# Optimization experiments

Hardware: AMD Instinct MI355X
Metric: run time of the kernel (lower is better)

Reference implementation:

```python
import jax, jax.numpy as jnp
import numpy as np

Z, Y, X = 41, 1024, 1024   # spatial_shape (z, y, x)
N = 300000                 # active voxels
C_IN, C_OUT, K = 32, 64, 3


def setup_inputs() -> dict:
    key = jax.random.key(0)
    k1, k2 = jax.random.split(key)
    # unique active voxel coordinates (spconv indices layout: [batch, z, y, x])
    rng = np.random.default_rng(0)
    lin = rng.choice(Z * Y * X, size=N, replace=False)
    z = lin // (Y * X)
    y = (lin // X) % Y
    x = lin % X
    indices = np.stack([np.zeros(N, np.int64), z, y, x], axis=1).astype(np.int32)
    features = jax.random.normal(k1, (N, C_IN), dtype=jnp.float32)
    fan_in = K * K * K * C_IN
    weight = jax.random.normal(k2, (K * K * K, C_IN, C_OUT), dtype=jnp.float32) / np.sqrt(fan_in)
    return {"features": features, "indices": jnp.asarray(indices), "weight": weight}


def reference(features, indices, weight):
    """Submanifold sparse 3D conv (SubMConv3d, k=3, pad=1, no bias).

    Output sites == input active sites. For each of the 27 kernel offsets:
    look up the neighbor voxel in a dense coordinate hash, gather its
    features, matmul with that offset's [C_in, C_out] weight slice, and
    accumulate (gather-matmul-scatter rulebook form).
    """
    n = features.shape[0]
    zc, yc, xc = indices[:, 1], indices[:, 2], indices[:, 3]
    lin = (zc * (Y * X) + yc * X + xc).astype(jnp.int32)
    # dense hash: linear voxel coord -> row in `features`, -1 if inactive
    grid = jnp.full((Z * Y * X,), -1, dtype=jnp.int32).at[lin].set(
        jnp.arange(n, dtype=jnp.int32))

    out = jnp.zeros((n, C_OUT), dtype=features.dtype)
    k = 0
    for dz in (-1, 0, 1):
        for dy in (-1, 0, 1):
            for dx in (-1, 0, 1):
                nz, ny, nx = zc + dz, yc + dy, xc + dx
                inb = ((nz >= 0) & (nz < Z) & (ny >= 0) & (ny < Y)
                       & (nx >= 0) & (nx < X))
                nlin = jnp.where(inb, nz * (Y * X) + ny * X + nx, 0)
                nidx = grid[nlin]                       # [N] row or -1
                mask = inb & (nidx >= 0)
                feat = features[jnp.where(mask, nidx, 0)]
                feat = feat * mask[:, None].astype(features.dtype)
                out = out + feat @ weight[k]            # [N,Cin]@[Cin,Cout]
                k += 1
    return out
```

## Files before the change

### kernel.cpp

```cpp
#include <hip/hip_runtime.h>
#include <hip/hip_fp16.h>


#define ZD 41
#define YD 1024
#define XD 1024

constexpr int CIN = 32;
constexpr int COUT = 64;
constexpr unsigned HASH_BITS = 20;
constexpr unsigned CAP = 1u << HASH_BITS;
constexpr unsigned GROUP_BITS = HASH_BITS - 3;
constexpr unsigned long long EMPTY = ~0ull;
constexpr unsigned NVOX = ZD * YD * XD;
constexpr unsigned NOCT = NVOX / 8;
constexpr unsigned BMWORDS = (NOCT + 31) / 32;
constexpr int PPW = 16;
constexpr int CAND_CAP = 96;
constexpr int HROWS = 48;
constexpr int WPACK_N = 27 * 4 * 64;

typedef _Float16 half2_t __attribute__((ext_vector_type(2)));
typedef _Float16 half8_t __attribute__((ext_vector_type(8)));
typedef __fp16 pk2_t __attribute__((ext_vector_type(2)));
typedef float floatx4 __attribute__((ext_vector_type(4)));

union H2U { pk2_t p; half2_t h; unsigned u; };
union H8U { half8_t v; half2_t h2[4]; pk2_t p2[4]; uint4 u4; };

__host__ __device__ constexpr unsigned pack6(int k) {
    return (unsigned)((k % 3) | (((k / 3) % 3) << 2) | ((k / 9) << 4));
}
__host__ __device__ constexpr unsigned cw_round(int t) {
    unsigned w = 0;
    for (int j4 = 0; j4 < 4; ++j4) {
        int off = 4 * t + j4;
        if (off < 26) {
            int k = off + (off >= 13);
            w |= pack6(k) << (6 * j4);
        }
    }
    return w;
}

__device__ __forceinline__ unsigned hash_slot(unsigned lin) {
    unsigned gh = ((lin >> 3) * 2654435761u) >> (32 - GROUP_BITS);
    return (gh << 3) | (lin & 7u);
}

__global__ void build_hash_kernel(const int4* __restrict__ idx, int n,
                                  unsigned long long* __restrict__ table,
                                  unsigned* __restrict__ bitmap,
                                  const float* __restrict__ weight,
                                  uint4* __restrict__ wpack) {
    int i = blockIdx.x * blockDim.x + threadIdx.x;
    if (i < WPACK_N) {
        int co = i & 63, g = (i >> 6) & 3, k = i >> 8;
        const float* b = weight + k * (CIN * COUT) + (8 * g) * COUT + co;
        H2U p0, p1, p2, p3;
        p0.p = __builtin_amdgcn_cvt_pkrtz(b[0 * COUT], b[1 * COUT]);
        p1.p = __builtin_amdgcn_cvt_pkrtz(b[2 * COUT], b[3 * COUT]);
        p2.p = __builtin_amdgcn_cvt_pkrtz(b[4 * COUT], b[5 * COUT]);
        p3.p = __builtin_amdgcn_cvt_pkrtz(b[6 * COUT], b[7 * COUT]);
        wpack[i] = make_uint4(p0.u, p1.u, p2.u, p3.u);
    }
    if (i >= n) return;
    int4 c = idx[i];
    unsigned lin = (unsigned)(c.y * (YD * XD) + c.z * XD + c.w);
    unsigned g = lin >> 3;
    atomicAnd(&bitmap[g >> 5], ~(1u << (g & 31u)));
    unsigned long long packed = ((unsigned long long)(unsigned)i << 32) | (unsigned long long)lin;
    unsigned h = hash_slot(lin);
    while (atomicCAS(&table[h], EMPTY, packed) != EMPTY) {
        h = (h + 1) & (CAP - 1);
    }
}

__device__ __forceinline__ int lookup(const unsigned long long* __restrict__ table,
                                      unsigned lin) {
    unsigned h = hash_slot(lin);
    while (true) {
        unsigned long long s = table[h];
        if (s == EMPTY) return -1;
        if ((unsigned)s == lin) return (int)(s >> 32);
        h = (h + 1) & (CAP - 1);
    }
}

__device__ __forceinline__ void fb_tap(const float* __restrict__ feat,
                                       const float* __restrict__ weight,
                                       float* __restrict__ acc,
                                       int ni, int pt, int k, int lane) {
    const float4* fr = (const float4*)(feat + (size_t)ni * CIN);
    const float* wk = weight + k * (CIN * COUT) + lane;
    float s0 = 0.f, s1 = 0.f, s2 = 0.f, s3 = 0.f;
#pragma unroll
    for (int q = 0; q < 8; ++q) {
        float4 f = fr[q];
        s0 = fmaf(f.x, wk[(4 * q + 0) * COUT], s0);
        s1 = fmaf(f.y, wk[(4 * q + 1) * COUT], s1);
        s2 = fmaf(f.z, wk[(4 * q + 2) * COUT], s2);
        s3 = fmaf(f.w, wk[(4 * q + 3) * COUT], s3);
    }
    acc[pt * COUT + lane] += (s0 + s1) + (s2 + s3);
}

__global__ __launch_bounds__(256, 4) void subm_conv_kernel(
    const float* __restrict__ feat, const int4* __restrict__ idx,
    const float* __restrict__ weight, const uint4* __restrict__ wpack,
    const unsigned long long* __restrict__ table,
    const unsigned* __restrict__ bitmap, float* __restrict__ out, int n) {
    __shared__ unsigned rows_l[4][HROWS * 16];
    __shared__ float accum_l[4][PPW * COUT];
    __shared__ unsigned long long cand_l[4][CAND_CAP];
    __shared__ unsigned hlist_l[4][HROWS];

    int wid = threadIdx.x >> 6;
    int lane = threadIdx.x & 63;
    int p0 = (blockIdx.x * 4 + wid) * PPW;
    if (p0 >= n) return;
    int np = min(PPW, n - p0);

    int pt = lane >> 2;
    int4 c = idx[p0 + (pt < np ? pt : 0)];

    int sh6 = (lane & 3) * 6;
    bool ptok = (pt < np);
    unsigned nlin_t[7];
    unsigned bmw[7];
    bool try_t[7];
#pragma unroll
    for (int t = 0; t < 7; ++t) {
        unsigned w = (cw_round(t) >> sh6) & 63u;
        int nz = c.y + (int)(w >> 4) - 1;
        int ny = c.z + (int)((w >> 2) & 3u) - 1;
        int nx = c.w + (int)(w & 3u) - 1;
        bool ok = ptok && (unsigned)nz < (unsigned)ZD && (unsigned)ny < (unsigned)YD &&
                  (unsigned)nx < (unsigned)XD;
        if (t == 6) ok = ok && ((lane & 3) < 2);
        unsigned nlin = ok ? ((((unsigned)nz << 10) + (unsigned)ny) << 10) + (unsigned)nx : 0u;
        nlin_t[t] = nlin;
        try_t[t] = ok;
        bmw[t] = ok ? bitmap[nlin >> 8] : ~0u;
    }

    int arow = lane & 15, aq = lane >> 4;
    int rowp = p0 + (arow < np ? arow : np - 1);
    float4 af0 = *(const float4*)(feat + (size_t)rowp * CIN + aq * 8);
    float4 af1 = *(const float4*)(feat + (size_t)rowp * CIN + aq * 8 + 4);
    H8U afrag;
    afrag.p2[0] = __builtin_amdgcn_cvt_pkrtz(af0.x, af0.y);
    afrag.p2[1] = __builtin_amdgcn_cvt_pkrtz(af0.z, af0.w);
    afrag.p2[2] = __builtin_amdgcn_cvt_pkrtz(af1.x, af1.y);
    afrag.p2[3] = __builtin_amdgcn_cvt_pkrtz(af1.z, af1.w);

    floatx4 cacc[4];
#pragma unroll
    for (int ch = 0; ch < 4; ++ch) {
        H8U bfrag;
        bfrag.u4 = wpack[(13 * 4 + aq) * 64 + ch * 16 + (lane & 15)];
        floatx4 z = {0.f, 0.f, 0.f, 0.f};
        cacc[ch] = __builtin_amdgcn_mfma_f32_16x16x32_f16(afrag.v, bfrag.v, z, 0, 0, 0);
    }
#pragma unroll
    for (int ch = 0; ch < 4; ++ch) {
#pragma unroll
        for (int r = 0; r < 4; ++r) {
            accum_l[wid][((lane >> 4) * 4 + r) * COUT + ch * 16 + (lane & 15)] = cacc[ch][r];
        }
    }

    int cbase = 0;
    unsigned ovmask = 0;
#pragma unroll
    for (int t = 0; t < 7; ++t) {
        unsigned nlin = nlin_t[t];
        bool candq = try_t[t] && !((bmw[t] >> ((nlin >> 3) & 31u)) & 1u);
        unsigned long long m = __ballot(candq);
        if (candq) {
            int r = cbase + __popcll(m & ((1ull << lane) - 1ull));
            int off = (lane & 3) + 4 * t;
            int k = off + (off >= 13);
            if (r < CAND_CAP) {
                cand_l[wid][r] = ((unsigned long long)(((unsigned)pt << 5) | (unsigned)k) << 32)
                                 | (unsigned long long)nlin;
            } else {
                ovmask |= 1u << t;
            }
        }
        cbase += __popcll(m);
    }
    int ncand = cbase < CAND_CAP ? cbase : CAND_CAP;
    __asm__ __volatile__("s_waitcnt lgkmcnt(0)" ::: "memory");

    int hitbase = 0;
    int hni[2];
    unsigned hmeta[2];
    bool hov[2] = {false, false};
#pragma unroll
    for (int sub = 0; sub < 2; ++sub) {
        int j = sub * 64 + lane;
        int ni = -1;
        unsigned meta = 0;
        if (j < ncand) {
            unsigned long long e = cand_l[wid][j];
            meta = (unsigned)(e >> 32);
            ni = lookup(table, (unsigned)e);
        }
        unsigned long long m = __ballot(ni >= 0);
        if (ni >= 0) {
            int hr = hitbase + __popcll(m & ((1ull << lane) - 1ull));
            if (hr < HROWS) {
                hlist_l[wid][hr] = ((unsigned)ni << 9) | meta;
            } else {
                hov[sub] = true; hni[sub] = ni; hmeta[sub] = meta;
            }
        }
        hitbase += __popcll(m);
    }
    int hits = hitbase < HROWS ? hitbase : HROWS;
    __asm__ __volatile__("s_waitcnt lgkmcnt(0)" ::: "memory");

    for (int e = lane; e < hits * 4; e += 64) {
        int r = e >> 2, s = e & 3;
        int ni = (int)(hlist_l[wid][r] >> 9);
        float4 u = *(const float4*)(feat + (size_t)ni * CIN + s * 8);
        float4 v = *(const float4*)(feat + (size_t)ni * CIN + s * 8 + 4);
        H2U q0, q1, q2, q3;
        q0.p = __builtin_amdgcn_cvt_pkrtz(u.x, u.y);
        q1.p = __builtin_amdgcn_cvt_pkrtz(u.z, u.w);
        q2.p = __builtin_amdgcn_cvt_pkrtz(v.x, v.y);
        q3.p = __builtin_amdgcn_cvt_pkrtz(v.z, v.w);
        *(uint4*)&rows_l[wid][r * 16 + s * 4] = make_uint4(q0.u, q1.u, q2.u, q3.u);
    }
    __asm__ __volatile__("s_waitcnt vmcnt(0) lgkmcnt(0)" ::: "memory");

    for (int j = 0; j < hits; ++j) {
        unsigned meta = hlist_l[wid][j] & 511u;
        int k = (int)(meta & 31u);
        int pt2 = (int)(meta >> 5);
        float s = 0.f;
#pragma unroll
        for (int g = 0; g < 4; ++g) {
            H8U fv, wv;
            fv.u4 = *(const uint4*)&rows_l[wid][j * 16 + g * 4];
            wv.u4 = wpack[(k * 4 + g) * 64 + lane];
            s = __builtin_amdgcn_fdot2(fv.h2[0], wv.h2[0], s, false);
            s = __builtin_amdgcn_fdot2(fv.h2[1], wv.h2[1], s, false);
            s = __builtin_amdgcn_fdot2(fv.h2[2], wv.h2[2], s, false);
            s = __builtin_amdgcn_fdot2(fv.h2[3], wv.h2[3], s, false);
        }
        accum_l[wid][pt2 * COUT + lane] += s;
    }

    if (__builtin_expect(cbase > CAND_CAP, 0)) {
#pragma unroll
        for (int t = 0; t < 7; ++t) {
            unsigned long long m = __ballot((ovmask >> t) & 1u);
            while (m) {
                int src = __ffsll((unsigned long long)m) - 1;
                m &= m - 1;
                unsigned nlin = __shfl(nlin_t[t], src);
                int pt2 = src >> 2;
                int off = (src & 3) + 4 * t;
                int k = off + (off >= 13);
                int ni = lookup(table, nlin);
                if (ni >= 0) fb_tap(feat, weight, accum_l[wid], ni, pt2, k, lane);
            }
        }
    }
    if (__builtin_expect(hitbase > HROWS, 0)) {
#pragma unroll
        for (int sub = 0; sub < 2; ++sub) {
            unsigned long long m = __ballot(hov[sub]);
            while (m) {
                int src = __ffsll((unsigned long long)m) - 1;
                m &= m - 1;
                int ni = __shfl(hni[sub], src);
                unsigned meta = (unsigned)__shfl((int)hmeta[sub], src);
                fb_tap(feat, weight, accum_l[wid], ni, (int)((meta >> 5) & 15u),
                       (int)(meta & 31u), lane);
            }
        }
    }
    __asm__ __volatile__("s_waitcnt lgkmcnt(0)" ::: "memory");

    for (int e = lane; e < np * 16; e += 64) {
        int g = e >> 4, cq = e & 15;
        floatx4 v = *(const floatx4*)&accum_l[wid][g * COUT + cq * 4];
        __builtin_nontemporal_store(v, (floatx4*)&out[(size_t)(p0 + g) * COUT + cq * 4]);
    }
}

extern "C" void kernel_launch(void* const* d_in, const int* in_sizes, int n_in,
                              void* d_out, int out_size, void* d_ws, size_t ws_size,
                              hipStream_t stream) {
    const float* feat   = (const float*)d_in[0];
    const int4*  idx    = (const int4*)d_in[1];
    const float* weight = (const float*)d_in[2];
    float* out = (float*)d_out;
    int n = in_sizes[0] / CIN;

    unsigned char* base = (unsigned char*)d_ws;
    unsigned long long* table = (unsigned long long*)base;
    unsigned* bitmap = (unsigned*)(base + (size_t)CAP * 8);
    uint4* wpack = (uint4*)(base + (size_t)CAP * 8 + (size_t)BMWORDS * 4);

    hipMemsetAsync(table, 0xFF, (size_t)CAP * 8 + (size_t)BMWORDS * 4, stream);

    int bwork = n > WPACK_N ? n : WPACK_N;
    int bblocks = (bwork + 255) / 256;
    build_hash_kernel<<<bblocks, 256, 0, stream>>>(idx, n, table, bitmap, weight, wpack);

    int ppb = 4 * PPW;
    int cblocks = (n + ppb - 1) / ppb;
    subm_conv_kernel<<<cblocks, 256, 0, stream>>>(feat, idx, weight, wpack, table,
                                                  bitmap, out, n);
}
```

Before: 184.0 us.

## Make conv kernel persistent and prefetch next group's coordinates and bitmap words

Converts the per-wave single-group kernel into a grid-stride persistent loop capped at a fixed block count. Coordinates and occupancy-bitmap words for the next group are loaded and computed while the current group does its hash lookups and gathers, hiding their latency. It also removes the vmcnt wait before the dot-product loop. The cap reduces resident waves per CU, which may lower latency hiding for the gather-heavy path, and adds register pressure from the carried prefetch state.

Result: slower. 209.3 us (+13.8%).

```diff
diff --git a/kernel.cpp b/kernel.cpp
--- a/kernel.cpp
+++ b/kernel.cpp
@@ -19,6 +19,7 @@
 constexpr int CAND_CAP = 96;
 constexpr int HROWS = 48;
 constexpr int WPACK_N = 27 * 4 * 64;
+constexpr int PERSIST_BLOCKS = 768;
 
 typedef _Float16 half2_t __attribute__((ext_vector_type(2)));
 typedef _Float16 half8_t __attribute__((ext_vector_type(8)));
@@ -117,178 +118,222 @@
 
     int wid = threadIdx.x >> 6;
     int lane = threadIdx.x & 63;
-    int p0 = (blockIdx.x * 4 + wid) * PPW;
-    if (p0 >= n) return;
-    int np = min(PPW, n - p0);
-
     int pt = lane >> 2;
-    int4 c = idx[p0 + (pt < np ? pt : 0)];
-
     int sh6 = (lane & 3) * 6;
-    bool ptok = (pt < np);
-    unsigned nlin_t[7];
-    unsigned bmw[7];
-    bool try_t[7];
-#pragma unroll
-    for (int t = 0; t < 7; ++t) {
-        unsigned w = (cw_round(t) >> sh6) & 63u;
-        int nz = c.y + (int)(w >> 4) - 1;
-        int ny = c.z + (int)((w >> 2) & 3u) - 1;
-        int nx = c.w + (int)(w & 3u) - 1;
-        bool ok = ptok && (unsigned)nz < (unsigned)ZD && (unsigned)ny < (unsigned)YD &&
-                  (unsigned)nx < (unsigned)XD;
-        if (t == 6) ok = ok && ((lane & 3) < 2);
-        unsigned nlin = ok ? ((((unsigned)nz << 10) + (unsigned)ny) << 10) + (unsigned)nx : 0u;
-        nlin_t[t] = nlin;
-        try_t[t] = ok;
-        bmw[t] = ok ? bitmap[nlin >> 8] : ~0u;
-    }
-
-    int arow = lane & 15, aq = lane >> 4;
-    int rowp = p0 + (arow < np ? arow : np - 1);
-    float4 af0 = *(const float4*)(feat + (size_t)rowp * CIN + aq * 8);
-    float4 af1 = *(const float4*)(feat + (size_t)rowp * CIN + aq * 8 + 4);
-    H8U afrag;
-    afrag.p2[0] = __builtin_amdgcn_cvt_pkrtz(af0.x, af0.y);
-    afrag.p2[1] = __builtin_amdgcn_cvt_pkrtz(af0.z, af0.w);
-    afrag.p2[2] = __builtin_amdgcn_cvt_pkrtz(af1.x, af1.y);
-    afrag.p2[3] = __builtin_amdgcn_cvt_pkrtz(af1.z, af1.w);
-
-    floatx4 cacc[4];
-#pragma unroll
-    for (int ch = 0; ch < 4; ++ch) {
-        H8U bfrag;
-        bfrag.u4 = wpack[(13 * 4 + aq) * 64 + ch * 16 + (lane & 15)];
-        floatx4 z = {0.f, 0.f, 0.f, 0.f};
-        cacc[ch] = __builtin_amdgcn_mfma_f32_16x16x32_f16(afrag.v, bfrag.v, z, 0, 0, 0);
-    }
-#pragma unroll
-    for (int ch = 0; ch < 4; ++ch) {
-#pragma unroll
-        for (int r = 0; r < 4; ++r) {
-            accum_l[wid][((lane >> 4) * 4 + r) * COUT + ch * 16 + (lane & 15)] = cacc[ch][r];
-        }
-    }
-
-    int cbase = 0;
-    unsigned ovmask = 0;
-#pragma unroll
-    for (int t = 0; t < 7; ++t) {
-        unsigned nlin = nlin_t[t];
-        bool candq = try_t[t] && !((bmw[t] >> ((nlin >> 3) & 31u)) & 1u);
-        unsigned long long m = __ballot(candq);
-        if (candq) {
-            int r = cbase + __popcll(m & ((1ull << lane) - 1ull));
-            int off = (lane & 3) + 4 * t;
-            int k = off + (off >= 13);
-            if (r < CAND_CAP) {
-                cand_l[wid][r] = ((unsigned long long)(((unsigned)pt << 5) | (unsigned)k) << 32)
-                                 | (unsigned long long)nlin;
-            } else {
-                ovmask |= 1u << t;
-            }
-        }
-        cbase += __popcll(m);
-    }
-    int ncand = cbase < CAND_CAP ? cbase : CAND_CAP;
-    __asm__ __volatile__("s_waitcnt lgkmcnt(0)" ::: "memory");
-
-    int hitbase = 0;
-    int hni[2];
-    unsigned hmeta[2];
-    bool hov[2] = {false, false};
-#pragma unroll
-    for (int sub = 0; sub < 2; ++sub) {
-        int j = sub * 64 + lane;
-        int ni = -1;
-        unsigned meta = 0;
-        if (j < ncand) {
-            unsigned long long e = cand_l[wid][j];
-            meta = (unsigned)(e >> 32);
-            ni = lookup(table, (unsigned)e);
-        }
-        unsigned long long m = __ballot(ni >= 0);
-        if (ni >= 0) {
-            int hr = hitbase + __popcll(m & ((1ull << lane) - 1ull));
-            if (hr < HROWS) {
-                hlist_l[wid][hr] = ((unsigned)ni << 9) | meta;
-            } else {
-                hov[sub] = true; hni[sub] = ni; hmeta[sub] = meta;
-            }
-        }
-        hitbase += __popcll(m);
-    }
-    int hits = hitbase < HROWS ? hitbase : HROWS;
-    __asm__ __volatile__("s_waitcnt lgkmcnt(0)" ::: "memory");
-
-    for (int e = lane; e < hits * 4; e += 64) {
-        int r = e >> 2, s = e & 3;
-        int ni = (int)(hlist_l[wid][r] >> 9);
-        float4 u = *(const float4*)(feat + (size_t)ni * CIN + s * 8);
-        float4 v = *(const float4*)(feat + (size_t)ni * CIN + s * 8 + 4);
-        H2U q0, q1, q2, q3;
-        q0.p = __builtin_amdgcn_cvt_pkrtz(u.x, u.y);
-        q1.p = __builtin_amdgcn_cvt_pkrtz(u.z, u.w);
-        q2.p = __builtin_amdgcn_cvt_pkrtz(v.x, v.y);
-        q3.p = __builtin_amdgcn_cvt_pkrtz(v.z, v.w);
-        *(uint4*)&rows_l[wid][r * 16 + s * 4] = make_uint4(q0.u, q1.u, q2.u, q3.u);
-    }
-    __asm__ __volatile__("s_waitcnt vmcnt(0) lgkmcnt(0)" ::: "memory");
-
-    for (int j = 0; j < hits; ++j) {
-        unsigned meta = hlist_l[wid][j] & 511u;
-        int k = (int)(meta & 31u);
-        int pt2 = (int)(meta >> 5);
-        float s = 0.f;
-#pragma unroll
-        for (int g = 0; g < 4; ++g) {
-            H8U fv, wv;
-            fv.u4 = *(const uint4*)&rows_l[wid][j * 16 + g * 4];
-            wv.u4 = wpack[(k * 4 + g) * 64 + lane];
-            s = __builtin_amdgcn_fdot2(fv.h2[0], wv.h2[0], s, false);
-            s = __builtin_amdgcn_fdot2(fv.h2[1], wv.h2[1], s, false);
-            s = __builtin_amdgcn_fdot2(fv.h2[2], wv.h2[2], s, false);
-            s = __builtin_amdgcn_fdot2(fv.h2[3], wv.h2[3], s, false);
-        }
-        accum_l[wid][pt2 * COUT + lane] += s;
-    }
-
-    if (__builtin_expect(cbase > CAND_CAP, 0)) {
+
+    int ngroups = (n + PPW - 1) / PPW;
+    int gstride = gridDim.x * 4;
+    int g = blockIdx.x * 4 + wid;
+    if (g >= ngroups) return;
+
+    unsigned nlin_n[7], bmw_n[7];
+    bool try_n[7];
+    {
+        int np0 = min(PPW, n - g * PPW);
+        int4 cc = idx[g * PPW + (pt < np0 ? pt : 0)];
+        bool ptok = (pt < np0);
 #pragma unroll
         for (int t = 0; t < 7; ++t) {
-            unsigned long long m = __ballot((ovmask >> t) & 1u);
-            while (m) {
-                int src = __ffsll((unsigned long long)m) - 1;
-                m &= m - 1;
-                unsigned nlin = __shfl(nlin_t[t], src);
-                int pt2 = src >> 2;
-                int off = (src & 3) + 4 * t;
+            unsigned w = (cw_round(t) >> sh6) & 63u;
+            int nz = cc.y + (int)(w >> 4) - 1;
+            int ny = cc.z + (int)((w >> 2) & 3u) - 1;
+            int nx = cc.w + (int)(w & 3u) - 1;
+            bool ok = ptok && (unsigned)nz < (unsigned)ZD && (unsigned)ny < (unsigned)YD &&
+                      (unsigned)nx < (unsigned)XD;
+            if (t == 6) ok = ok && ((lane & 3) < 2);
+            unsigned nl = ok ? ((((unsigned)nz << 10) + (unsigned)ny) << 10) + (unsigned)nx : 0u;
+            nlin_n[t] = nl;
+            try_n[t] = ok;
+            bmw_n[t] = ok ? bitmap[nl >> 8] : ~0u;
+        }
+    }
+
+    for (; g < ngroups; g += gstride) {
+        int p0 = g * PPW;
+        int np = min(PPW, n - p0);
+
+        unsigned nlin_t[7], bmw[7];
+        bool try_t[7];
+#pragma unroll
+        for (int t = 0; t < 7; ++t) {
+            nlin_t[t] = nlin_n[t];
+            bmw[t] = bmw_n[t];
+            try_t[t] = try_n[t];
+        }
+
+        int gn = g + gstride;
+        bool has_next = gn < ngroups;
+        int np_nx = has_next ? min(PPW, n - gn * PPW) : np;
+        int nsrc = has_next ? (gn * PPW + (pt < np_nx ? pt : 0)) : p0;
+        int4 cnext = idx[nsrc];
+
+        int arow = lane & 15, aq = lane >> 4;
+        int rowp = p0 + (arow < np ? arow : np - 1);
+        float4 af0 = *(const float4*)(feat + (size_t)rowp * CIN + aq * 8);
+        float4 af1 = *(const float4*)(feat + (size_t)rowp * CIN + aq * 8 + 4);
+        H8U afrag;
+        afrag.p2[0] = __builtin_amdgcn_cvt_pkrtz(af0.x, af0.y);
+        afrag.p2[1] = __builtin_amdgcn_cvt_pkrtz(af0.z, af0.w);
+        afrag.p2[2] = __builtin_amdgcn_cvt_pkrtz(af1.x, af1.y);
+        afrag.p2[3] = __builtin_amdgcn_cvt_pkrtz(af1.z, af1.w);
+
+        floatx4 cacc[4];
+#pragma unroll
+        for (int ch = 0; ch < 4; ++ch) {
+            H8U bfrag;
+            bfrag.u4 = wpack[(13 * 4 + aq) * 64 + ch * 16 + (lane & 15)];
+            floatx4 z = {0.f, 0.f, 0.f, 0.f};
+            cacc[ch] = __builtin_amdgcn_mfma_f32_16x16x32_f16(afrag.v, bfrag.v, z, 0, 0, 0);
+        }
+#pragma unroll
+        for (int ch = 0; ch < 4; ++ch) {
+#pragma unroll
+            for (int r = 0; r < 4; ++r) {
+                accum_l[wid][((lane >> 4) * 4 + r) * COUT + ch * 16 + (lane & 15)] =
+                    cacc[ch][r];
+            }
+        }
+
+        int cbase = 0;
+        unsigned ovmask = 0;
+#pragma unroll
+        for (int t = 0; t < 7; ++t) {
+            unsigned nlin = nlin_t[t];
+            bool candq = try_t[t] && !((bmw[t] >> ((nlin >> 3) & 31u)) & 1u);
+            unsigned long long m = __ballot(candq);
+            if (candq) {
+                int r = cbase + __popcll(m & ((1ull << lane) - 1ull));
+                int off = (lane & 3) + 4 * t;
                 int k = off + (off >= 13);
-                int ni = lookup(table, nlin);
-                if (ni >= 0) fb_tap(feat, weight, accum_l[wid], ni, pt2, k, lane);
-            }
-        }
-    }
-    if (__builtin_expect(hitbase > HROWS, 0)) {
+                if (r < CAND_CAP) {
+                    cand_l[wid][r] =
+                        ((unsigned long long)(((unsigned)pt << 5) | (unsigned)k) << 32)
+                        | (unsigned long long)nlin;
+                } else {
+                    ovmask |= 1u << t;
+                }
+            }
+            cbase += __popcll(m);
+        }
+        int ncand = cbase < CAND_CAP ? cbase : CAND_CAP;
+        __asm__ __volatile__("s_waitcnt lgkmcnt(0)" ::: "memory");
+
+        int hitbase = 0;
+        int hni[2];
+        unsigned hmeta[2];
+        bool hov[2] = {false, false};
 #pragma unroll
         for (int sub = 0; sub < 2; ++sub) {
-            unsigned long long m = __ballot(hov[sub]);
-            while (m) {
-                int src = __ffsll((unsigned long long)m) - 1;
-                m &= m - 1;
-                int ni = __shfl(hni[sub], src);
-                unsigned meta = (unsigned)__shfl((int)hmeta[sub], src);
-                fb_tap(feat, weight, accum_l[wid], ni, (int)((meta >> 5) & 15u),
-                       (int)(meta & 31u), lane);
-            }
-        }
-    }
-    __asm__ __volatile__("s_waitcnt lgkmcnt(0)" ::: "memory");
-
-    for (int e = lane; e < np * 16; e += 64) {
-        int g = e >> 4, cq = e & 15;
-        floatx4 v = *(const floatx4*)&accum_l[wid][g * COUT + cq * 4];
-        __builtin_nontemporal_store(v, (floatx4*)&out[(size_t)(p0 + g) * COUT + cq * 4]);
+            int j = sub * 64 + lane;
+            int ni = -1;
+            unsigned meta = 0;
+            if (j < ncand) {
+                unsigned long long e = cand_l[wid][j];
+                meta = (unsigned)(e >> 32);
+                ni = lookup(table, (unsigned)e);
+            }
+            unsigned long long m = __ballot(ni >= 0);
+            if (ni >= 0) {
+                int hr = hitbase + __popcll(m & ((1ull << lane) - 1ull));
+                if (hr < HROWS) {
+                    hlist_l[wid][hr] = ((unsigned)ni << 9) | meta;
+                } else {
+                    hov[sub] = true; hni[sub] = ni; hmeta[sub] = meta;
+                }
+            }
+            hitbase += __popcll(m);
+        }
+        int hits = hitbase < HROWS ? hitbase : HROWS;
+        __asm__ __volatile__("s_waitcnt lgkmcnt(0)" ::: "memory");
+
+        {
+            bool ptok_n = has_next && (pt < np_nx);
+#pragma unroll
+            for (int t = 0; t < 7; ++t) {
+                unsigned w = (cw_round(t) >> sh6) & 63u;
+                int nz = cnext.y + (int)(w >> 4) - 1;
+                int ny = cnext.z + (int)((w >> 2) & 3u) - 1;
+                int nx = cnext.w + (int)(w & 3u) - 1;
+                bool ok = ptok_n && (unsigned)nz < (unsigned)ZD &&
+                          (unsigned)ny < (unsigned)YD && (unsigned)nx < (unsigned)XD;
+                if (t == 6) ok = ok && ((lane & 3) < 2);
+                unsigned nl = ok ? ((((unsigned)nz << 10) + (unsigned)ny) << 10) + (unsigned)nx
+                                 : 0u;
+                nlin_n[t] = nl;
+                try_n[t] = ok;
+                bmw_n[t] = ok ? bitmap[nl >> 8] : ~0u;
+            }
+        }
+
+        for (int e = lane; e < hits * 4; e += 64) {
+            int r = e >> 2, s = e & 3;
+            int ni = (int)(hlist_l[wid][r] >> 9);
+            float4 u = *(const float4*)(feat + (size_t)ni * CIN + s * 8);
+            float4 v = *(const float4*)(feat + (size_t)ni * CIN + s * 8 + 4);
+            H2U q0, q1, q2, q3;
+            q0.p = __builtin_amdgcn_cvt_pkrtz(u.x, u.y);
+            q1.p = __builtin_amdgcn_cvt_pkrtz(u.z, u.w);
+            q2.p = __builtin_amdgcn_cvt_pkrtz(v.x, v.y);
+            q3.p = __builtin_amdgcn_cvt_pkrtz(v.z, v.w);
+            *(uint4*)&rows_l[wid][r * 16 + s * 4] = make_uint4(q0.u, q1.u, q2.u, q3.u);
+        }
+        __asm__ __volatile__("s_waitcnt lgkmcnt(0)" ::: "memory");
+
+        for (int j = 0; j < hits; ++j) {
+            unsigned meta = hlist_l[wid][j] & 511u;
+            int k = (int)(meta & 31u);
+            int pt2 = (int)(meta >> 5);
+            float s = 0.f;
+#pragma unroll
+            for (int gg = 0; gg < 4; ++gg) {
+                H8U fv, wv;
+                fv.u4 = *(const uint4*)&rows_l[wid][j * 16 + gg * 4];
+                wv.u4 = wpack[(k * 4 + gg) * 64 + lane];
+                s = __builtin_amdgcn_fdot2(fv.h2[0], wv.h2[0], s, false);
+                s = __builtin_amdgcn_fdot2(fv.h2[1], wv.h2[1], s, false);
+                s = __builtin_amdgcn_fdot2(fv.h2[2], wv.h2[2], s, false);
+                s = __builtin_amdgcn_fdot2(fv.h2[3], wv.h2[3], s, false);
+            }
+            accum_l[wid][pt2 * COUT + lane] += s;
+        }
+
+        if (__builtin_expect(cbase > CAND_CAP, 0)) {
+#pragma unroll
+            for (int t = 0; t < 7; ++t) {
+                unsigned long long m = __ballot((ovmask >> t) & 1u);
+                while (m) {
+                    int src = __ffsll((unsigned long long)m) - 1;
+                    m &= m - 1;
+                    unsigned nlin = __shfl(nlin_t[t], src);
+                    int pt2 = src >> 2;
+                    int off = (src & 3) + 4 * t;
+                    int k = off + (off >= 13);
+                    int ni = lookup(table, nlin);
+                    if (ni >= 0) fb_tap(feat, weight, accum_l[wid], ni, pt2, k, lane);
+                }
+            }
+        }
+        if (__builtin_expect(hitbase > HROWS, 0)) {
+#pragma unroll
+            for (int sub = 0; sub < 2; ++sub) {
+                unsigned long long m = __ballot(hov[sub]);
+                while (m) {
+                    int src = __ffsll((unsigned long long)m) - 1;
+                    m &= m - 1;
+                    int ni = __shfl(hni[sub], src);
+                    unsigned meta = (unsigned)__shfl((int)hmeta[sub], src);
+                    fb_tap(feat, weight, accum_l[wid], ni, (int)((meta >> 5) & 15u),
+                           (int)(meta & 31u), lane);
+                }
+            }
+        }
+        __asm__ __volatile__("s_waitcnt lgkmcnt(0)" ::: "memory");
+
+        for (int e = lane; e < np * 16; e += 64) {
+            int gr = e >> 4, cq = e & 15;
+            floatx4 v = *(const floatx4*)&accum_l[wid][gr * COUT + cq * 4];
+            __builtin_nontemporal_store(v, (floatx4*)&out[(size_t)(p0 + gr) * COUT + cq * 4]);
+        }
     }
 }
 
@@ -312,8 +357,9 @@
     int bblocks = (bwork + 255) / 256;
     build_hash_kernel<<<bblocks, 256, 0, stream>>>(idx, n, table, bitmap, weight, wpack);
 
-    int ppb = 4 * PPW;
-    int cblocks = (n + ppb - 1) / ppb;
+    int ngroups = (n + PPW - 1) / PPW;
+    int cblocks = (ngroups + 3) / 4;
+    if (cblocks > PERSIST_BLOCKS) cblocks = PERSIST_BLOCKS;
     subm_conv_kernel<<<cblocks, 256, 0, stream>>>(feat, idx, weight, wpack, table,
                                                   bitmap, out, n);
 }
```

## Use per-voxel occupancy bitmap and do hash lookups in place without candidate compaction

Applied to the files above, without the earlier changes.

The occupancy bitmap goes from one bit per 2x2x2 octant to one bit per voxel, so a set bit means a neighbour really exists. Because of that, the kernel no longer compacts candidates into shared memory and then runs a second compaction pass. Each lane looks up its own exact hits directly and writes them to the hit list by ballot rank, and the second overflow fallback is removed. The trade-offs are a bitmap eight times larger to clear and read, which hits cache less often, and up to seven serialized, divergent lookup rounds per wave instead of two coalesced ones.

Result: slower. 189.9 us (+3.2%).

```diff
diff --git a/kernel.cpp b/kernel.cpp
--- a/kernel.cpp
+++ b/kernel.cpp
@@ -13,10 +13,8 @@
 constexpr unsigned GROUP_BITS = HASH_BITS - 3;
 constexpr unsigned long long EMPTY = ~0ull;
 constexpr unsigned NVOX = ZD * YD * XD;
-constexpr unsigned NOCT = NVOX / 8;
-constexpr unsigned BMWORDS = (NOCT + 31) / 32;
+constexpr unsigned BMWORDS = (NVOX + 31) / 32;
 constexpr int PPW = 16;
-constexpr int CAND_CAP = 96;
 constexpr int HROWS = 48;
 constexpr int WPACK_N = 27 * 4 * 64;
 
@@ -67,8 +65,7 @@
     if (i >= n) return;
     int4 c = idx[i];
     unsigned lin = (unsigned)(c.y * (YD * XD) + c.z * XD + c.w);
-    unsigned g = lin >> 3;
-    atomicAnd(&bitmap[g >> 5], ~(1u << (g & 31u)));
+    atomicAnd(&bitmap[lin >> 5], ~(1u << (lin & 31u)));
     unsigned long long packed = ((unsigned long long)(unsigned)i << 32) | (unsigned long long)lin;
     unsigned h = hash_slot(lin);
     while (atomicCAS(&table[h], EMPTY, packed) != EMPTY) {
@@ -112,7 +109,6 @@
     const unsigned* __restrict__ bitmap, float* __restrict__ out, int n) {
     __shared__ unsigned rows_l[4][HROWS * 16];
     __shared__ float accum_l[4][PPW * COUT];
-    __shared__ unsigned long long cand_l[4][CAND_CAP];
     __shared__ unsigned hlist_l[4][HROWS];
 
     int wid = threadIdx.x >> 6;
@@ -141,7 +137,7 @@
         unsigned nlin = ok ? ((((unsigned)nz << 10) + (unsigned)ny) << 10) + (unsigned)nx : 0u;
         nlin_t[t] = nlin;
         try_t[t] = ok;
-        bmw[t] = ok ? bitmap[nlin >> 8] : ~0u;
+        bmw[t] = ok ? bitmap[nlin >> 5] : ~0u;
     }
 
     int arow = lane & 15, aq = lane >> 4;
@@ -171,54 +167,34 @@
     }
 
     int cbase = 0;
-    unsigned ovmask = 0;
+    bool c_val[7];
+    int c_rank[7];
 #pragma unroll
     for (int t = 0; t < 7; ++t) {
         unsigned nlin = nlin_t[t];
-        bool candq = try_t[t] && !((bmw[t] >> ((nlin >> 3) & 31u)) & 1u);
+        bool candq = try_t[t] && !((bmw[t] >> (nlin & 31u)) & 1u);
         unsigned long long m = __ballot(candq);
-        if (candq) {
-            int r = cbase + __popcll(m & ((1ull << lane) - 1ull));
+        c_val[t] = candq;
+        c_rank[t] = cbase + (int)__popcll(m & ((1ull << lane) - 1ull));
+        cbase += (int)__popcll(m);
+    }
+
+    unsigned ovmask = 0;
+#pragma unroll
+    for (int t = 0; t < 7; ++t) {
+        if (c_val[t]) {
             int off = (lane & 3) + 4 * t;
             int k = off + (off >= 13);
-            if (r < CAND_CAP) {
-                cand_l[wid][r] = ((unsigned long long)(((unsigned)pt << 5) | (unsigned)k) << 32)
-                                 | (unsigned long long)nlin;
+            int ni = lookup(table, nlin_t[t]);
+            int r = c_rank[t];
+            if (r < HROWS && ni >= 0) {
+                hlist_l[wid][r] = ((unsigned)ni << 9) | ((unsigned)pt << 5) | (unsigned)k;
             } else {
                 ovmask |= 1u << t;
             }
         }
-        cbase += __popcll(m);
-    }
-    int ncand = cbase < CAND_CAP ? cbase : CAND_CAP;
-    __asm__ __volatile__("s_waitcnt lgkmcnt(0)" ::: "memory");
-
-    int hitbase = 0;
-    int hni[2];
-    unsigned hmeta[2];
-    bool hov[2] = {false, false};
-#pragma unroll
-    for (int sub = 0; sub < 2; ++sub) {
-        int j = sub * 64 + lane;
-        int ni = -1;
-        unsigned meta = 0;
-        if (j < ncand) {
-            unsigned long long e = cand_l[wid][j];
-            meta = (unsigned)(e >> 32);
-            ni = lookup(table, (unsigned)e);
-        }
-        unsigned long long m = __ballot(ni >= 0);
-        if (ni >= 0) {
-            int hr = hitbase + __popcll(m & ((1ull << lane) - 1ull));
-            if (hr < HROWS) {
-                hlist_l[wid][hr] = ((unsigned)ni << 9) | meta;
-            } else {
-                hov[sub] = true; hni[sub] = ni; hmeta[sub] = meta;
-            }
-        }
-        hitbase += __popcll(m);
-    }
-    int hits = hitbase < HROWS ? hitbase : HROWS;
+    }
+    int hits = cbase < HROWS ? cbase : HROWS;
     __asm__ __volatile__("s_waitcnt lgkmcnt(0)" ::: "memory");
 
     for (int e = lane; e < hits * 4; e += 64) {
@@ -253,7 +229,7 @@
         accum_l[wid][pt2 * COUT + lane] += s;
     }
 
-    if (__builtin_expect(cbase > CAND_CAP, 0)) {
+    if (__builtin_expect(cbase > HROWS, 0)) {
 #pragma unroll
         for (int t = 0; t < 7; ++t) {
             unsigned long long m = __ballot((ovmask >> t) & 1u);
@@ -269,20 +245,6 @@
             }
         }
     }
-    if (__builtin_expect(hitbase > HROWS, 0)) {
-#pragma unroll
-        for (int sub = 0; sub < 2; ++sub) {
-            unsigned long long m = __ballot(hov[sub]);
-            while (m) {
-                int src = __ffsll((unsigned long long)m) - 1;
-                m &= m - 1;
-                int ni = __shfl(hni[sub], src);
-                unsigned meta = (unsigned)__shfl((int)hmeta[sub], src);
-                fb_tap(feat, weight, accum_l[wid], ni, (int)((meta >> 5) & 15u),
-                       (int)(meta & 31u), lane);
-            }
-        }
-    }
     __asm__ __volatile__("s_waitcnt lgkmcnt(0)" ::: "memory");
 
     for (int e = lane; e < np * 16; e += 64) {
```
